# Kernel optimization log

Measured on AMD Instinct MI355X. Metric: run time of the kernel, lower is better.

Reference implementation:

```python
import jax, jax.numpy as jnp
import numpy as np

EPS = 1e-12
ALPHA = 0.2  # LeakyReLU negative slope
N_NODES = 100000
N_EDGES = 1600000
F = 128
H = 8

def setup_inputs() -> dict:
    key = jax.random.key(0)
    k1, k2, k3, k4 = jax.random.split(key, 4)
    x = jax.random.normal(k1, (N_NODES, F), dtype=jnp.float32)
    row = jax.random.randint(k2, (N_EDGES,), 0, N_NODES, dtype=jnp.int32)
    col = jax.random.randint(k3, (N_EDGES,), 0, N_NODES, dtype=jnp.int32)
    # xavier_uniform with gain=1.414 on [H, 2F]
    limit = 1.414 * np.sqrt(6.0 / (H + 2 * F))
    aa = jax.random.uniform(k4, (H, 2 * F), dtype=jnp.float32, minval=-limit, maxval=limit)
    return {"x": x, "row": row, "col": col, "aa": aa}

def reference(x, row, col, aa):
    # e = leakyrelu(aa @ cat(x[row], x[col], dim=1).T)  -> [H, E]
    # Split aa so per-node scores are computed once, then gathered per edge
    # (identical math, avoids materializing the [E, 2F] concat).
    a_src, a_dst = aa[:, :F], aa[:, F:]          # [H, F] each
    s_src = x @ a_src.T                           # [N, H]
    s_dst = x @ a_dst.T                           # [N, H]
    e = s_src[row] + s_dst[col]                   # [E, H]
    e = jnp.where(e > 0, e, ALPHA * e)            # LeakyReLU
    # scatter_softmax over edges grouped by row (per head)
    m = jax.ops.segment_max(e, row, num_segments=N_NODES)  # [N, H]
    m = jnp.where(jnp.isfinite(m), m, 0.0)        # empty segments -> -inf; neutralize
    ex = jnp.exp(e - m[row])                      # [E, H]
    s = jax.ops.segment_sum(ex, row, num_segments=N_NODES)  # [N, H]
    a = ex / (s[row] + EPS)                       # [E, H]
    return a.T                                    # [H, E] to match torch layout
```

## Files before the change

### kernel.cpp

```cpp
#include <hip/hip_runtime.h>

constexpr int N_NODES = 100000;
constexpr int N_EDGES = 1600000;
constexpr int F = 128;
constexpr int H = 8;
constexpr float ALPHA = 0.2f;
constexpr float EPSF = 1e-12f;

constexpr int PSHIFT = 8;
constexpr int PN = 1 << PSHIFT;
constexpr int NPART = (N_NODES + PN - 1) / PN;
constexpr int MAXPART = 5120;
constexpr int EPB = 4096;
constexpr int OCAP = 4096;
constexpr int NPAIR = H / 2;

__global__ void k1_scores(const float* __restrict__ x, const float* __restrict__ aa,
                          float* __restrict__ srn, float* __restrict__ sd,
                          float2* __restrict__ sd2) {
    __shared__ float sa[H * 2 * F];
    for (int i = threadIdx.x; i < H * 2 * F; i += blockDim.x) sa[i] = aa[i];
    __syncthreads();
    int node = blockIdx.x * blockDim.x + threadIdx.x;
    if (node >= N_NODES) return;
    const float4* xr = reinterpret_cast<const float4*>(x + (size_t)node * F);
    float accs[H], accd[H];
#pragma unroll
    for (int h = 0; h < H; ++h) { accs[h] = 0.f; accd[h] = 0.f; }
    for (int f4 = 0; f4 < F / 4; ++f4) {
        float4 xv = xr[f4];
#pragma unroll
        for (int h = 0; h < H; ++h) {
            float4 av = *reinterpret_cast<const float4*>(&sa[h * 2 * F + 4 * f4]);
            float4 bv = *reinterpret_cast<const float4*>(&sa[h * 2 * F + F + 4 * f4]);
            accs[h] += xv.x * av.x + xv.y * av.y + xv.z * av.z + xv.w * av.w;
            accd[h] += xv.x * bv.x + xv.y * bv.y + xv.z * bv.z + xv.w * bv.w;
        }
    }
    float4* os = reinterpret_cast<float4*>(srn + (size_t)node * 16);
    os[0] = make_float4(accs[0], accs[1], accs[2], accs[3]);
    os[1] = make_float4(accs[4], accs[5], accs[6], accs[7]);
    float4* od = reinterpret_cast<float4*>(sd + (size_t)node * H);
    od[0] = make_float4(accd[0], accd[1], accd[2], accd[3]);
    od[1] = make_float4(accd[4], accd[5], accd[6], accd[7]);
#pragma unroll
    for (int pi = 0; pi < NPAIR; ++pi)
        sd2[(size_t)pi * N_NODES + node] = make_float2(accd[2 * pi], accd[2 * pi + 1]);
}

__global__ void __launch_bounds__(1024)
kA_part(const int* __restrict__ row, const int* __restrict__ col,
        int* __restrict__ gcnt, unsigned* __restrict__ part,
        int* __restrict__ ocnt, int2* __restrict__ olist) {
    __shared__ int hist[NPART];
    __shared__ int base[NPART];
    const int t = threadIdx.x;
    const int e0 = blockIdx.x * EPB;
    for (int p = t; p < NPART; p += 1024) hist[p] = 0;
    __syncthreads();
    for (int k = 0; k < EPB / 1024; ++k) {
        int i = e0 + k * 1024 + t;
        if (i < N_EDGES) atomicAdd(&hist[row[i] >> PSHIFT], 1);
    }
    __syncthreads();
    for (int p = t; p < NPART; p += 1024) {
        int h = hist[p];
        base[p] = h ? atomicAdd(&gcnt[p], h) : 0;
        hist[p] = 0;
    }
    __syncthreads();
    for (int k = 0; k < EPB / 1024; ++k) {
        int i = e0 + k * 1024 + t;
        if (i < N_EDGES) {
            int r = row[i], c = col[i];
            int p = r >> PSHIFT;
            int slot = base[p] + atomicAdd(&hist[p], 1);
            unsigned pk = ((unsigned)(r & (PN - 1)) << 17) | (unsigned)c;
            if (slot < MAXPART) {
                part[(size_t)p * MAXPART + slot] = pk;
            } else {
                int q = atomicAdd(ocnt, 1);
                if (q < OCAP) olist[q] = make_int2(p, (int)pk);
            }
        }
    }
}

__global__ void __launch_bounds__(1024)
kB_sum(const float* __restrict__ sd, const unsigned* __restrict__ part,
       const int* __restrict__ gcnt, const int* __restrict__ ocnt,
       const int2* __restrict__ olist, const float* __restrict__ srn,
       float4* __restrict__ spn) {
    __shared__ unsigned plist[MAXPART];
    __shared__ unsigned sorted_c[MAXPART];
    __shared__ int hist[PN];
    __shared__ int off[PN + 1];
    __shared__ int cur[PN];
    __shared__ float ssrc[PN * H];
    const int p = blockIdx.x;
    const int t = threadIdx.x;
    const int nbase = p << PSHIFT;

    for (int i = t; i < PN; i += 1024) hist[i] = 0;
    for (int j = t; j < PN * H; j += 1024) {
        int n = nbase + (j >> 3);
        ssrc[j] = (n < N_NODES) ? srn[(size_t)n * 16 + (j & 7)] : 0.f;
    }
    __syncthreads();

    int cnt = gcnt[p]; if (cnt > MAXPART) cnt = MAXPART;
    const unsigned* pp = part + (size_t)p * MAXPART;

    for (int i = t; i < cnt; i += 1024) {
        unsigned pk = pp[i];
        plist[i] = pk;
        atomicAdd(&hist[pk >> 17], 1);
    }
    __syncthreads();

    for (int d = 1; d < PN; d <<= 1) {
        int add = 0;
        if (t >= d && t < PN) add = hist[t - d];
        __syncthreads();
        if (t < PN) hist[t] += add;
        __syncthreads();
    }
    if (t < PN) off[t + 1] = hist[t];
    if (t == 0) off[0] = 0;
    __syncthreads();
    if (t < PN) cur[t] = off[t];
    __syncthreads();

    for (int i = t; i < cnt; i += 1024) {
        unsigned pk = plist[i];
        int rl = (int)(pk >> 17);
        int slot = atomicAdd(&cur[rl], 1);
        sorted_c[slot] = pk & 0x1FFFFu;
    }
    __syncthreads();

    int mo = *ocnt; if (mo > OCAP) mo = OCAP;
    {
        int nl = t >> 2, pi = t & 3;
        int node = nbase + nl;
        int k0 = off[nl], k1e = off[nl + 1];
        float s0 = ssrc[nl * 8 + 2 * pi];
        float s1 = ssrc[nl * 8 + 2 * pi + 1];
        float a0 = 0.f, a1 = 0.f;
        for (int k = k0; k < k1e; ++k) {
            int c = (int)sorted_c[k];
            float2 d = *reinterpret_cast<const float2*>(&sd[(size_t)c * H + 2 * pi]);
            float e0 = s0 + d.x; e0 = e0 > 0.f ? e0 : ALPHA * e0;
            float e1 = s1 + d.y; e1 = e1 > 0.f ? e1 : ALPHA * e1;
            a0 += __expf(e0); a1 += __expf(e1);
        }
        for (int j = 0; j < mo; ++j) {
            int2 oe = olist[j];
            if (oe.x == p && (int)(((unsigned)oe.y) >> 17) == nl) {
                int c = oe.y & 0x1FFFF;
                float2 d = *reinterpret_cast<const float2*>(&sd[(size_t)c * H + 2 * pi]);
                float e0 = s0 + d.x; e0 = e0 > 0.f ? e0 : ALPHA * e0;
                float e1 = s1 + d.y; e1 = e1 > 0.f ? e1 : ALPHA * e1;
                a0 += __expf(e0); a1 += __expf(e1);
            }
        }
        if (node < N_NODES)
            spn[(size_t)pi * N_NODES + node] =
                make_float4(s0, s1, 1.f / (a0 + EPSF), 1.f / (a1 + EPSF));
    }
}

__global__ void k4p(const int* __restrict__ row, const int* __restrict__ col,
                    const float4* __restrict__ spn, const float2* __restrict__ sd2,
                    float* __restrict__ out) {
    int i = blockIdx.x * blockDim.x + threadIdx.x;
    if (i >= N_EDGES) return;
    int pi = blockIdx.y;
    int r = row[i], c = col[i];
    float4 q = spn[(size_t)pi * N_NODES + r];
    float2 d = sd2[(size_t)pi * N_NODES + c];
    float e0 = q.x + d.x; e0 = e0 > 0.f ? e0 : ALPHA * e0;
    float e1 = q.y + d.y; e1 = e1 > 0.f ? e1 : ALPHA * e1;
    out[(size_t)(2 * pi) * N_EDGES + i]     = __expf(e0) * q.z;
    out[(size_t)(2 * pi + 1) * N_EDGES + i] = __expf(e1) * q.w;
}

__global__ void kz_zero_sums(float* __restrict__ srn) {
    int t = blockIdx.x * blockDim.x + threadIdx.x;
    if (t >= N_NODES * H) return;
    srn[(size_t)(t >> 3) * 16 + 8 + (t & 7)] = 0.f;
}

__global__ void k3nm_sum(const float* __restrict__ srn_ro, const float* __restrict__ s_dst,
                         const int* __restrict__ row, const int* __restrict__ col,
                         float* __restrict__ srn) {
    int i = blockIdx.x * blockDim.x + threadIdx.x;
    if (i >= N_EDGES) return;
    int r = row[i], c = col[i];
    const float4* sr = reinterpret_cast<const float4*>(srn_ro + (size_t)r * 16);
    float4 a0 = sr[0], a1 = sr[1];
    const float4* sc = reinterpret_cast<const float4*>(s_dst + (size_t)c * H);
    float4 b0 = sc[0], b1 = sc[1];
    float ev[H] = {a0.x + b0.x, a0.y + b0.y, a0.z + b0.z, a0.w + b0.w,
                   a1.x + b1.x, a1.y + b1.y, a1.z + b1.z, a1.w + b1.w};
#pragma unroll
    for (int h = 0; h < H; ++h) {
        float e = ev[h] > 0.f ? ev[h] : ALPHA * ev[h];
        atomicAdd(&srn[(size_t)r * 16 + 8 + h], __expf(e));
    }
}

__global__ void k_inv(float* __restrict__ srn) {
    int t = blockIdx.x * blockDim.x + threadIdx.x;
    if (t >= N_NODES * H) return;
    int n = t >> 3, h = t & 7;
    float s = srn[(size_t)n * 16 + 8 + h];
    srn[(size_t)n * 16 + 8 + h] = 1.0f / (s + EPSF);
}

__global__ void k4_out(const int* __restrict__ row, const int* __restrict__ col,
                       const float* __restrict__ srn, const float* __restrict__ s_dst,
                       float* __restrict__ out) {
    int i = blockIdx.x * blockDim.x + threadIdx.x;
    if (i >= N_EDGES) return;
    int r = row[i], c = col[i];
    const float4* sr = reinterpret_cast<const float4*>(srn + (size_t)r * 16);
    float4 a0 = sr[0], a1 = sr[1], r0 = sr[2], r1 = sr[3];
    const float4* sc = reinterpret_cast<const float4*>(s_dst + (size_t)c * H);
    float4 b0 = sc[0], b1 = sc[1];
    float ev[H] = {a0.x + b0.x, a0.y + b0.y, a0.z + b0.z, a0.w + b0.w,
                   a1.x + b1.x, a1.y + b1.y, a1.z + b1.z, a1.w + b1.w};
    float rv[H] = {r0.x, r0.y, r0.z, r0.w, r1.x, r1.y, r1.z, r1.w};
#pragma unroll
    for (int h = 0; h < H; ++h) {
        float e = ev[h] > 0.f ? ev[h] : ALPHA * ev[h];
        out[(size_t)h * N_EDGES + i] = __expf(e) * rv[h];
    }
}

extern "C" void kernel_launch(void* const* d_in, const int* in_sizes, int n_in,
                              void* d_out, int out_size, void* d_ws, size_t ws_size,
                              hipStream_t stream) {
    const float* x   = (const float*)d_in[0];
    const int*   row = (const int*)d_in[1];
    const int*   col = (const int*)d_in[2];
    const float* aa  = (const float*)d_in[3];
    float* out = (float*)d_out;

    float*    srn  = (float*)d_ws;
    float*    sd   = srn + (size_t)N_NODES * 16;
    float4*   spn  = (float4*)(sd + (size_t)N_NODES * H);
    float2*   sd2  = (float2*)(spn + (size_t)NPAIR * N_NODES);
    unsigned* part = (unsigned*)(sd2 + (size_t)NPAIR * N_NODES);
    int*      gcnt = (int*)(part + (size_t)NPART * MAXPART);
    int*      ocnt = gcnt + NPART;
    int2*     olist = (int2*)(ocnt + 16);

    const size_t need_full = ((size_t)N_NODES * (16 + 8 + 16 + 8) + (size_t)NPART * MAXPART
                              + NPART + 16 + 2 * OCAP) * 4;
    const size_t need_min  = (size_t)N_NODES * (16 + 8) * 4;

    const int B = 256;
    const int GE = (N_EDGES + B - 1) / B;
    const int GN = (N_NODES + B - 1) / B;

    k1_scores<<<GN, B, 0, stream>>>(x, aa, srn, sd, sd2);

    if (ws_size >= need_full) {
        hipMemsetAsync(gcnt, 0, (size_t)(NPART + 16) * sizeof(int), stream);
        kA_part<<<(N_EDGES + EPB - 1) / EPB, 1024, 0, stream>>>(row, col, gcnt, part, ocnt, olist);
        kB_sum<<<NPART, 1024, 0, stream>>>(sd, part, gcnt, ocnt, olist, srn, spn);
        dim3 g4(GE, NPAIR);
        k4p<<<g4, B, 0, stream>>>(row, col, spn, sd2, out);
    } else if (ws_size >= need_min) {
        kz_zero_sums<<<(N_NODES * H + B - 1) / B, B, 0, stream>>>(srn);
        k3nm_sum<<<GE, B, 0, stream>>>(srn, sd, row, col, srn);
        k_inv<<<(N_NODES * H + B - 1) / B, B, 0, stream>>>(srn);
        k4_out<<<GE, B, 0, stream>>>(row, col, srn, sd, out);
    }
}
```

Before: 222.6 us.

## Replace per-pair output kernel with single two-edge-per-thread output pass

```diff
diff --git a/kernel.cpp b/kernel.cpp
--- a/kernel.cpp
+++ b/kernel.cpp
@@ -13,11 +13,9 @@
 constexpr int MAXPART = 5120;
 constexpr int EPB = 4096;
 constexpr int OCAP = 4096;
-constexpr int NPAIR = H / 2;
 
 __global__ void k1_scores(const float* __restrict__ x, const float* __restrict__ aa,
-                          float* __restrict__ srn, float* __restrict__ sd,
-                          float2* __restrict__ sd2) {
+                          float* __restrict__ srn, float* __restrict__ sd) {
     __shared__ float sa[H * 2 * F];
     for (int i = threadIdx.x; i < H * 2 * F; i += blockDim.x) sa[i] = aa[i];
     __syncthreads();
@@ -43,9 +41,6 @@
     float4* od = reinterpret_cast<float4*>(sd + (size_t)node * H);
     od[0] = make_float4(accd[0], accd[1], accd[2], accd[3]);
     od[1] = make_float4(accd[4], accd[5], accd[6], accd[7]);
-#pragma unroll
-    for (int pi = 0; pi < NPAIR; ++pi)
-        sd2[(size_t)pi * N_NODES + node] = make_float2(accd[2 * pi], accd[2 * pi + 1]);
 }
 
 __global__ void __launch_bounds__(1024)
@@ -89,8 +84,7 @@
 __global__ void __launch_bounds__(1024)
 kB_sum(const float* __restrict__ sd, const unsigned* __restrict__ part,
        const int* __restrict__ gcnt, const int* __restrict__ ocnt,
-       const int2* __restrict__ olist, const float* __restrict__ srn,
-       float4* __restrict__ spn) {
+       const int2* __restrict__ olist, float* __restrict__ srn) {
     __shared__ unsigned plist[MAXPART];
     __shared__ unsigned sorted_c[MAXPART];
     __shared__ int hist[PN];
@@ -147,7 +141,25 @@
         float s0 = ssrc[nl * 8 + 2 * pi];
         float s1 = ssrc[nl * 8 + 2 * pi + 1];
         float a0 = 0.f, a1 = 0.f;
-        for (int k = k0; k < k1e; ++k) {
+        int k = k0;
+        for (; k + 4 <= k1e; k += 4) {
+            int c0 = (int)sorted_c[k],     c1 = (int)sorted_c[k + 1];
+            int c2 = (int)sorted_c[k + 2], c3 = (int)sorted_c[k + 3];
+            float2 d0 = *reinterpret_cast<const float2*>(&sd[(size_t)c0 * H + 2 * pi]);
+            float2 d1 = *reinterpret_cast<const float2*>(&sd[(size_t)c1 * H + 2 * pi]);
+            float2 d2 = *reinterpret_cast<const float2*>(&sd[(size_t)c2 * H + 2 * pi]);
+            float2 d3 = *reinterpret_cast<const float2*>(&sd[(size_t)c3 * H + 2 * pi]);
+            float e;
+            e = s0 + d0.x; e = e > 0.f ? e : ALPHA * e; a0 += __expf(e);
+            e = s1 + d0.y; e = e > 0.f ? e : ALPHA * e; a1 += __expf(e);
+            e = s0 + d1.x; e = e > 0.f ? e : ALPHA * e; a0 += __expf(e);
+            e = s1 + d1.y; e = e > 0.f ? e : ALPHA * e; a1 += __expf(e);
+            e = s0 + d2.x; e = e > 0.f ? e : ALPHA * e; a0 += __expf(e);
+            e = s1 + d2.y; e = e > 0.f ? e : ALPHA * e; a1 += __expf(e);
+            e = s0 + d3.x; e = e > 0.f ? e : ALPHA * e; a0 += __expf(e);
+            e = s1 + d3.y; e = e > 0.f ? e : ALPHA * e; a1 += __expf(e);
+        }
+        for (; k < k1e; ++k) {
             int c = (int)sorted_c[k];
             float2 d = *reinterpret_cast<const float2*>(&sd[(size_t)c * H + 2 * pi]);
             float e0 = s0 + d.x; e0 = e0 > 0.f ? e0 : ALPHA * e0;
@@ -164,25 +176,42 @@
                 a0 += __expf(e0); a1 += __expf(e1);
             }
         }
-        if (node < N_NODES)
-            spn[(size_t)pi * N_NODES + node] =
-                make_float4(s0, s1, 1.f / (a0 + EPSF), 1.f / (a1 + EPSF));
-    }
-}
-
-__global__ void k4p(const int* __restrict__ row, const int* __restrict__ col,
-                    const float4* __restrict__ spn, const float2* __restrict__ sd2,
-                    float* __restrict__ out) {
-    int i = blockIdx.x * blockDim.x + threadIdx.x;
-    if (i >= N_EDGES) return;
-    int pi = blockIdx.y;
-    int r = row[i], c = col[i];
-    float4 q = spn[(size_t)pi * N_NODES + r];
-    float2 d = sd2[(size_t)pi * N_NODES + c];
-    float e0 = q.x + d.x; e0 = e0 > 0.f ? e0 : ALPHA * e0;
-    float e1 = q.y + d.y; e1 = e1 > 0.f ? e1 : ALPHA * e1;
-    out[(size_t)(2 * pi) * N_EDGES + i]     = __expf(e0) * q.z;
-    out[(size_t)(2 * pi + 1) * N_EDGES + i] = __expf(e1) * q.w;
+        if (node < N_NODES) {
+            srn[(size_t)node * 16 + 8 + 2 * pi]     = 1.f / (a0 + EPSF);
+            srn[(size_t)node * 16 + 8 + 2 * pi + 1] = 1.f / (a1 + EPSF);
+        }
+    }
+}
+
+__global__ void __launch_bounds__(256)
+k4_out(const int* __restrict__ row, const int* __restrict__ col,
+       const float* __restrict__ srn, const float* __restrict__ sd,
+       float* __restrict__ out) {
+    int i0 = (blockIdx.x * blockDim.x + threadIdx.x) * 2;
+    if (i0 >= N_EDGES) return;
+    int2 rr = *reinterpret_cast<const int2*>(&row[i0]);
+    int2 cc = *reinterpret_cast<const int2*>(&col[i0]);
+    const float4* srA = reinterpret_cast<const float4*>(srn + (size_t)rr.x * 16);
+    const float4* srB = reinterpret_cast<const float4*>(srn + (size_t)rr.y * 16);
+    const float4* scA = reinterpret_cast<const float4*>(sd + (size_t)cc.x * H);
+    const float4* scB = reinterpret_cast<const float4*>(sd + (size_t)cc.y * H);
+    float4 sA0 = srA[0], sA1 = srA[1], rA0 = srA[2], rA1 = srA[3];
+    float4 sB0 = srB[0], sB1 = srB[1], rB0 = srB[2], rB1 = srB[3];
+    float4 dA0 = scA[0], dA1 = scA[1];
+    float4 dB0 = scB[0], dB1 = scB[1];
+    float eA[H] = {sA0.x + dA0.x, sA0.y + dA0.y, sA0.z + dA0.z, sA0.w + dA0.w,
+                   sA1.x + dA1.x, sA1.y + dA1.y, sA1.z + dA1.z, sA1.w + dA1.w};
+    float eB[H] = {sB0.x + dB0.x, sB0.y + dB0.y, sB0.z + dB0.z, sB0.w + dB0.w,
+                   sB1.x + dB1.x, sB1.y + dB1.y, sB1.z + dB1.z, sB1.w + dB1.w};
+    float vA[H] = {rA0.x, rA0.y, rA0.z, rA0.w, rA1.x, rA1.y, rA1.z, rA1.w};
+    float vB[H] = {rB0.x, rB0.y, rB0.z, rB0.w, rB1.x, rB1.y, rB1.z, rB1.w};
+#pragma unroll
+    for (int h = 0; h < H; ++h) {
+        float a = eA[h] > 0.f ? eA[h] : ALPHA * eA[h];
+        float b = eB[h] > 0.f ? eB[h] : ALPHA * eB[h];
+        float2 o = make_float2(__expf(a) * vA[h], __expf(b) * vB[h]);
+        *reinterpret_cast<float2*>(&out[(size_t)h * N_EDGES + i0]) = o;
+    }
 }
 
 __global__ void kz_zero_sums(float* __restrict__ srn) {
@@ -218,26 +247,6 @@
     srn[(size_t)n * 16 + 8 + h] = 1.0f / (s + EPSF);
 }
 
-__global__ void k4_out(const int* __restrict__ row, const int* __restrict__ col,
-                       const float* __restrict__ srn, const float* __restrict__ s_dst,
-                       float* __restrict__ out) {
-    int i = blockIdx.x * blockDim.x + threadIdx.x;
-    if (i >= N_EDGES) return;
-    int r = row[i], c = col[i];
-    const float4* sr = reinterpret_cast<const float4*>(srn + (size_t)r * 16);
-    float4 a0 = sr[0], a1 = sr[1], r0 = sr[2], r1 = sr[3];
-    const float4* sc = reinterpret_cast<const float4*>(s_dst + (size_t)c * H);
-    float4 b0 = sc[0], b1 = sc[1];
-    float ev[H] = {a0.x + b0.x, a0.y + b0.y, a0.z + b0.z, a0.w + b0.w,
-                   a1.x + b1.x, a1.y + b1.y, a1.z + b1.z, a1.w + b1.w};
-    float rv[H] = {r0.x, r0.y, r0.z, r0.w, r1.x, r1.y, r1.z, r1.w};
-#pragma unroll
-    for (int h = 0; h < H; ++h) {
-        float e = ev[h] > 0.f ? ev[h] : ALPHA * ev[h];
-        out[(size_t)h * N_EDGES + i] = __expf(e) * rv[h];
-    }
-}
-
 extern "C" void kernel_launch(void* const* d_in, const int* in_sizes, int n_in,
                               void* d_out, int out_size, void* d_ws, size_t ws_size,
                               hipStream_t stream) {
@@ -249,33 +258,30 @@
 
     float*    srn  = (float*)d_ws;
     float*    sd   = srn + (size_t)N_NODES * 16;
-    float4*   spn  = (float4*)(sd + (size_t)N_NODES * H);
-    float2*   sd2  = (float2*)(spn + (size_t)NPAIR * N_NODES);
-    unsigned* part = (unsigned*)(sd2 + (size_t)NPAIR * N_NODES);
+    unsigned* part = (unsigned*)(sd + (size_t)N_NODES * H);
     int*      gcnt = (int*)(part + (size_t)NPART * MAXPART);
     int*      ocnt = gcnt + NPART;
     int2*     olist = (int2*)(ocnt + 16);
 
-    const size_t need_full = ((size_t)N_NODES * (16 + 8 + 16 + 8) + (size_t)NPART * MAXPART
-                              + NPART + 16 + 2 * OCAP) * 4;
-    const size_t need_min  = (size_t)N_NODES * (16 + 8) * 4;
+    const size_t need_b = ((size_t)N_NODES * 24 + (size_t)NPART * MAXPART
+                           + NPART + 16 + 2 * OCAP) * 4;
 
     const int B = 256;
-    const int GE = (N_EDGES + B - 1) / B;
-    const int GN = (N_NODES + B - 1) / B;
-
-    k1_scores<<<GN, B, 0, stream>>>(x, aa, srn, sd, sd2);
-
-    if (ws_size >= need_full) {
+    const int GE  = (N_EDGES + B - 1) / B;
+    const int GE2 = (N_EDGES + 2 * B - 1) / (2 * B);
+    const int GN  = (N_NODES + B - 1) / B;
+
+    k1_scores<<<GN, B, 0, stream>>>(x, aa, srn, sd);
+
+    if (ws_size >= need_b) {
         hipMemsetAsync(gcnt, 0, (size_t)(NPART + 16) * sizeof(int), stream);
         kA_part<<<(N_EDGES + EPB - 1) / EPB, 1024, 0, stream>>>(row, col, gcnt, part, ocnt, olist);
-        kB_sum<<<NPART, 1024, 0, stream>>>(sd, part, gcnt, ocnt, olist, srn, spn);
-        dim3 g4(GE, NPAIR);
-        k4p<<<g4, B, 0, stream>>>(row, col, spn, sd2, out);
-    } else if (ws_size >= need_min) {
+        kB_sum<<<NPART, 1024, 0, stream>>>(sd, part, gcnt, ocnt, olist, srn);
+    } else {
         kz_zero_sums<<<(N_NODES * H + B - 1) / B, B, 0, stream>>>(srn);
         k3nm_sum<<<GE, B, 0, stream>>>(srn, sd, row, col, srn);
         k_inv<<<(N_NODES * H + B - 1) / B, B, 0, stream>>>(srn);
-        k4_out<<<GE, B, 0, stream>>>(row, col, srn, sd, out);
-    }
-}
+    }
+
+    k4_out<<<GE2, B, 0, stream>>>(row, col, srn, sd, out);
+}
```

New measurement: 214.7 us. 1.04x faster.
